# Performance work log

Measured on AMD Instinct MI355X. Metric: run time of the kernel, lower is better.

## Reference

```python
import jax, jax.numpy as jnp
import numpy as np

B, L, D = 32768, 256, 16  # batch, chain length, bond dim; physical dim d=2


def setup_inputs() -> dict:
    key = jax.random.key(0)
    k_phi, k_first, k_mid, k_last = jax.random.split(key, 4)
    scale = 1.0 / np.sqrt(2.0 * D)  # variance-preserving chain
    phi_batch = jax.random.normal(k_phi, (B, L, 2), dtype=jnp.float32)
    core_first = jax.random.normal(k_first, (2, D), dtype=jnp.float32) * scale
    cores_mid = jax.random.normal(k_mid, (L - 2, D, 2, D), dtype=jnp.float32) * scale
    core_last = jax.random.normal(k_last, (D, 2), dtype=jnp.float32) * scale
    out_bias = jnp.zeros((), dtype=jnp.float32)
    return {
        "phi_batch": phi_batch,
        "core_first": core_first,
        "cores_mid": cores_mid,
        "core_last": core_last,
        "out_bias": out_bias,
    }


def reference(phi_batch, core_first, cores_mid, core_last, out_bias):
    # MPS / tensor-train contraction, batched over samples.
    # Each sample contracts feature vectors phi[i] (len-2) into the physical
    # index of core i, then chains the resulting D x D matrices via a
    # left-to-right bond-space matvec (what cotengra would find per-sample).
    # v0: [B, D] = phi[:,0] contracted with first core [2, D]
    v0 = jnp.einsum("bp,pd->bd", phi_batch[:, 0], core_first)

    # middle features, scan-major layout: [L-2, B, 2]
    phis_mid = jnp.swapaxes(phi_batch[:, 1:-1], 0, 1)

    def step(v, xs):
        phi_t, core = xs  # phi_t: [B, 2], core: [D, 2, D]
        # contract bond then physical index; never materialize [B, D, D]
        u = jnp.einsum("bq,qpr->bpr", v, core)   # [B, 2, D]
        v_new = jnp.einsum("bp,bpr->br", phi_t, u)  # [B, D]
        return v_new, None

    v, _ = jax.lax.scan(step, v0, (phis_mid, cores_mid))

    # close the chain with last core [D, 2] and last feature [B, 2]
    out = jnp.einsum("bq,qp,bp->b", v, core_last, phi_batch[:, -1])
    return out + out_bias
```

## Files before the change

### kernel.cpp

```cpp
#include <hip/hip_runtime.h>
#include <stdint.h>


typedef short  bf16x8 __attribute__((ext_vector_type(8)));
typedef float  f32x4  __attribute__((ext_vector_type(4)));
typedef int    i32x4  __attribute__((ext_vector_type(4)));
typedef unsigned int u32;

#define NPF 64
#define NPB 63
#define BWD_OFF (NPF*4*64)
#define NCHUNK 32

#define PACK_HI(hi, lo) ((int)__builtin_amdgcn_perm((u32)(hi), (u32)(lo), 0x07060302u))

__device__ __forceinline__ u32 rne_bump(u32 u){ return u + 0x7FFFu + ((u >> 16) & 1u); }

__device__ __forceinline__ void async16(const void* g, void* l){
  __builtin_amdgcn_global_load_lds(
    (const __attribute__((address_space(1))) u32*)(uintptr_t)g,
    (__attribute__((address_space(3))) u32*)(uintptr_t)l, 16, 0, 0);
}

__global__ void build_pair_frags(const float* __restrict__ cm, i32x4* __restrict__ ws)
{
  __shared__ float Ca[512], Cb[512];
  const int bid = blockIdx.x;
  const bool fwd = bid < NPF;
  const int j  = fwd ? bid : bid - NPF;
  const int ta = fwd ? 2*j     : 252 - 2*j;
  const int tb = fwd ? 2*j + 1 : 253 - 2*j;
  {
    const float* A = cm + ta*512;
    const float* B = cm + tb*512;
    for (int i = threadIdx.x; i < 512; i += 256){ Ca[i] = A[i]; Cb[i] = B[i]; }
  }
  __syncthreads();
  const int f    = threadIdx.x >> 6;
  const int lane = threadIdx.x & 63;
  const int m    = lane & 15;
  const int g    = lane >> 4;
  const int p    = f >> 1, q = f & 1;
  u32 hi[4], lo[4];
  #pragma unroll
  for (int x = 0; x < 4; ++x){
    const int cq = 4*g + x;
    float acc = 0.f;
    #pragma unroll
    for (int r = 0; r < 16; ++r){
      const float a = fwd ? Ca[cq*32 + p*16 + r] : Ca[m*32 + p*16 + r];
      const float b = fwd ? Cb[r*32 + q*16 + m]  : Cb[r*32 + q*16 + cq];
      acc = fmaf(a, b, acc);
    }
    const u32 u  = __float_as_uint(acc);
    const u32 aa = rne_bump(u);
    const float hf = __uint_as_float(aa & 0xFFFF0000u);
    const u32 bb = rne_bump(__float_as_uint(acc - hf));
    hi[x] = aa >> 16; lo[x] = bb >> 16;
  }
  i32x4 w;
  w[0] = (int)(hi[0] | (hi[1] << 16));
  w[1] = (int)(hi[2] | (hi[3] << 16));
  w[2] = (int)(lo[0] | (lo[1] << 16));
  w[3] = (int)(lo[2] | (lo[3] << 16));
  ws[(fwd ? 0 : BWD_OFF) + (j*4 + f)*64 + lane] = w;
}

__global__ __launch_bounds__(256, 4) void mps_chain(
  const float* __restrict__ phi,
  const float* __restrict__ core_first,
  const float* __restrict__ core_last,
  const float* __restrict__ bias,
  const i32x4* __restrict__ ws,
  float* __restrict__ out)
{
  const int lane = threadIdx.x & 63;
  const int wv   = threadIdx.x >> 6;
  const int b0   = blockIdx.x * 32;
  const int n    = lane & 15;
  const int g    = lane >> 4;
  const int half = wv & 1;
  const int s_in = half*16 + n;
  const bool isFwd = (wv < 2);
  const int dirIdx = isFwd ? 0 : 1;

  __shared__ i32x4 frag[2][2][2][4][64];
  __shared__ float phL[2][2][2][4][16][4];

  const float* phiRow = phi + (size_t)(b0 + s_in) * 512;

  const float* phiDma = phi + (size_t)(b0 + 16*half + (lane & 15)) * 512
                            + (lane >> 4) * 4;
  const i32x4* wsD = isFwd ? ws : (ws + BWD_OFF);

  auto issue_dma = [&](int cn, int buf){
    int pr = 2*cn + half;
    if (!isFwd && pr > NPB-1) pr = NPB-1;
    const i32x4* base = wsD + pr*4*64 + lane;
    #pragma unroll
    for (int f = 0; f < 4; ++f)
      async16(base + f*64, &frag[dirIdx][buf][half][f][0]);
    const int W = isFwd ? 4*cn : (248 - 4*cn);
    async16(phiDma + 2*W, &phL[dirIdx][buf][half][0][0][0]);
  };

  float v[4];
  i32x4 bfr;

  auto make_bfrag = [&](){
    const u32 u0 = __float_as_uint(v[0]), u1 = __float_as_uint(v[1]);
    const u32 u2 = __float_as_uint(v[2]), u3 = __float_as_uint(v[3]);
    const float l0 = v[0] - __uint_as_float(u0 & 0xFFFF0000u);
    const float l1 = v[1] - __uint_as_float(u1 & 0xFFFF0000u);
    const float l2 = v[2] - __uint_as_float(u2 & 0xFFFF0000u);
    const float l3 = v[3] - __uint_as_float(u3 & 0xFFFF0000u);
    bfr[0] = PACK_HI(u1, u0);
    bfr[1] = PACK_HI(u3, u2);
    bfr[2] = PACK_HI(__float_as_uint(l1), __float_as_uint(l0));
    bfr[3] = PACK_HI(__float_as_uint(l3), __float_as_uint(l2));
  };

  auto pair_step = [&](const i32x4& G0, const i32x4& G1, const i32x4& G2,
                       const i32x4& G3, float2 cA, float2 cB){
    const float c00 = cA.x*cB.x, c01 = cA.x*cB.y;
    const float c10 = cA.y*cB.x, c11 = cA.y*cB.y;
    i32x4 sw; sw[0]=bfr[2]; sw[1]=bfr[3]; sw[2]=bfr[0]; sw[3]=bfr[1];
    const bf16x8 bh = __builtin_bit_cast(bf16x8, bfr);
    const bf16x8 bs = __builtin_bit_cast(bf16x8, sw);
    const f32x4 z = {0.f,0.f,0.f,0.f};
    f32x4 a00 = __builtin_amdgcn_mfma_f32_16x16x32_bf16(__builtin_bit_cast(bf16x8,G0), bh, z, 0,0,0);
    a00 = __builtin_amdgcn_mfma_f32_16x16x32_bf16(__builtin_bit_cast(bf16x8,G0), bs, a00, 0,0,0);
    f32x4 a01 = __builtin_amdgcn_mfma_f32_16x16x32_bf16(__builtin_bit_cast(bf16x8,G1), bh, z, 0,0,0);
    a01 = __builtin_amdgcn_mfma_f32_16x16x32_bf16(__builtin_bit_cast(bf16x8,G1), bs, a01, 0,0,0);
    f32x4 a10 = __builtin_amdgcn_mfma_f32_16x16x32_bf16(__builtin_bit_cast(bf16x8,G2), bh, z, 0,0,0);
    a10 = __builtin_amdgcn_mfma_f32_16x16x32_bf16(__builtin_bit_cast(bf16x8,G2), bs, a10, 0,0,0);
    f32x4 a11 = __builtin_amdgcn_mfma_f32_16x16x32_bf16(__builtin_bit_cast(bf16x8,G3), bh, z, 0,0,0);
    a11 = __builtin_amdgcn_mfma_f32_16x16x32_bf16(__builtin_bit_cast(bf16x8,G3), bs, a11, 0,0,0);
    #pragma unroll
    for (int i2 = 0; i2 < 4; ++i2)
      v[i2] = c00*a00[i2] + c01*a01[i2] + c10*a10[i2] + c11*a11[i2];
    make_bfrag();
  };

  if (isFwd){
    const float2 ph0 = *(const float2*)phiRow;
    #pragma unroll
    for (int reg = 0; reg < 4; ++reg){
      const int r = g*4 + reg;
      v[reg] = ph0.x * core_first[r] + ph0.y * core_first[16 + r];
    }
  } else {
    const float2 phL2 = *(const float2*)(phiRow + 510);
    #pragma unroll
    for (int reg = 0; reg < 4; ++reg){
      const int r = g*4 + reg;
      v[reg] = phL2.x * core_last[2*r] + phL2.y * core_last[2*r + 1];
    }
  }
  make_bfrag();

  issue_dma(0, 0);
  __syncthreads();

  #pragma unroll 1
  for (int c = 0; c < NCHUNK; ++c){
    const int buf = c & 1;
    if (c + 1 < NCHUNK) issue_dma(c + 1, buf ^ 1);

    const float* pb = &phL[dirIdx][buf][half][0][n][0];
    const float2 xA0 = *(const float2*)(pb + (isFwd ?   2 : 130));
    const float2 xB0 = *(const float2*)(pb + (isFwd ?  64 : 192));
    const float2 xA1 = *(const float2*)(pb + 66);
    const float2 xB1 = *(const float2*)(pb + 128);

    {
      const i32x4 G0 = frag[dirIdx][buf][0][0][lane];
      const i32x4 G1 = frag[dirIdx][buf][0][1][lane];
      const i32x4 G2 = frag[dirIdx][buf][0][2][lane];
      const i32x4 G3 = frag[dirIdx][buf][0][3][lane];
      pair_step(G0, G1, G2, G3, xA0, xB0);
    }
    if (isFwd || (2*c + 1) < NPB){
      const i32x4 G0 = frag[dirIdx][buf][1][0][lane];
      const i32x4 G1 = frag[dirIdx][buf][1][1][lane];
      const i32x4 G2 = frag[dirIdx][buf][1][2][lane];
      const i32x4 G3 = frag[dirIdx][buf][1][3][lane];
      pair_step(G0, G1, G2, G3, xA1, xB1);
    }
    __syncthreads();
  }

  float* red = (float*)&frag[0][0][0][0][0];
  *(float4*)&red[(dirIdx*32 + s_in)*20 + 4*g] =
      make_float4(v[0], v[1], v[2], v[3]);
  __syncthreads();
  if (threadIdx.x < 32){
    const int s = threadIdx.x;
    float acc = bias[0];
    #pragma unroll
    for (int qq = 0; qq < 16; ++qq)
      acc += red[s*20 + qq] * red[(32 + s)*20 + qq];
    out[b0 + s] = acc;
  }
}

extern "C" void kernel_launch(void* const* d_in, const int* in_sizes, int n_in,
                              void* d_out, int out_size, void* d_ws, size_t ws_size,
                              hipStream_t stream)
{
  const float* phi  = (const float*)d_in[0];
  const float* cf   = (const float*)d_in[1];
  const float* cm   = (const float*)d_in[2];
  const float* cl   = (const float*)d_in[3];
  const float* bias = (const float*)d_in[4];
  i32x4* ws = (i32x4*)d_ws;

  build_pair_frags<<<NPF + NPB, 256, 0, stream>>>(cm, ws);
  mps_chain<<<1024, 256, 0, stream>>>(phi, cf, cl, bias, ws, (float*)d_out);
}
```

Before: 138.0 us.

## Load phi features directly to registers with two-stage prefetch and manual waitcnt

Removes the LDS staging buffer for phi features. Each lane now reads float4 phi values straight from global memory into registers, prefetched two chunks ahead, with a carry register handling the odd/even feature alignment. The pair-fragment DMA becomes a simple pointer walk, and the workspace is padded with extra pairs so that overrun reads stay in bounds. The full __syncthreads is replaced by an explicit vmcnt waitcnt plus s_barrier so the register prefetches can remain in flight across iterations. The trade-offs are fragile hand-written waitcnt encodings, extra build blocks that read cores outside their valid range, and more register pressure.

New measurement: 143.1 us. 1.04x slower.

```diff
diff --git a/kernel.cpp b/kernel.cpp
--- a/kernel.cpp
+++ b/kernel.cpp
@@ -9,7 +9,8 @@
 
 #define NPF 64
 #define NPB 63
-#define BWD_OFF (NPF*4*64)
+#define NP_ALLOC 66
+#define BWD_OFF (NP_ALLOC*4*64)
 #define NCHUNK 32
 
 #define PACK_HI(hi, lo) ((int)__builtin_amdgcn_perm((u32)(hi), (u32)(lo), 0x07060302u))
@@ -26,8 +27,8 @@
 {
   __shared__ float Ca[512], Cb[512];
   const int bid = blockIdx.x;
-  const bool fwd = bid < NPF;
-  const int j  = fwd ? bid : bid - NPF;
+  const bool fwd = bid < NP_ALLOC;
+  const int j  = fwd ? bid : bid - NP_ALLOC;
   const int ta = fwd ? 2*j     : 252 - 2*j;
   const int tb = fwd ? 2*j + 1 : 253 - 2*j;
   {
@@ -85,27 +86,17 @@
   const int dirIdx = isFwd ? 0 : 1;
 
   __shared__ i32x4 frag[2][2][2][4][64];
-  __shared__ float phL[2][2][2][4][16][4];
 
   const float* phiRow = phi + (size_t)(b0 + s_in) * 512;
-
-  const float* phiDma = phi + (size_t)(b0 + 16*half + (lane & 15)) * 512
-                            + (lane >> 4) * 4;
   const i32x4* wsD = isFwd ? ws : (ws + BWD_OFF);
 
-  auto issue_dma = [&](int cn, int buf){
-    int pr = 2*cn + half;
-    if (!isFwd && pr > NPB-1) pr = NPB-1;
-    const i32x4* base = wsD + pr*4*64 + lane;
-    #pragma unroll
-    for (int f = 0; f < 4; ++f)
-      async16(base + f*64, &frag[dirIdx][buf][half][f][0]);
-    const int W = isFwd ? 4*cn : (248 - 4*cn);
-    async16(phiDma + 2*W, &phL[dirIdx][buf][half][0][0][0]);
-  };
+  const i32x4* dmaSrc = wsD + half*256 + lane;
+  i32x4* const dst0 = &frag[dirIdx][0][half][0][0];
+  i32x4* const dst1 = &frag[dirIdx][1][half][0][0];
 
   float v[4];
   i32x4 bfr;
+  const f32x4 z = {0.f,0.f,0.f,0.f};
 
   auto make_bfrag = [&](){
     const u32 u0 = __float_as_uint(v[0]), u1 = __float_as_uint(v[1]);
@@ -120,14 +111,13 @@
     bfr[3] = PACK_HI(__float_as_uint(l3), __float_as_uint(l2));
   };
 
-  auto pair_step = [&](const i32x4& G0, const i32x4& G1, const i32x4& G2,
-                       const i32x4& G3, float2 cA, float2 cB){
+  auto pair_step = [&](const i32x4* fr, float2 cA, float2 cB){
+    const i32x4 G0 = fr[0], G1 = fr[64], G2 = fr[128], G3 = fr[192];
     const float c00 = cA.x*cB.x, c01 = cA.x*cB.y;
     const float c10 = cA.y*cB.x, c11 = cA.y*cB.y;
     i32x4 sw; sw[0]=bfr[2]; sw[1]=bfr[3]; sw[2]=bfr[0]; sw[3]=bfr[1];
     const bf16x8 bh = __builtin_bit_cast(bf16x8, bfr);
     const bf16x8 bs = __builtin_bit_cast(bf16x8, sw);
-    const f32x4 z = {0.f,0.f,0.f,0.f};
     f32x4 a00 = __builtin_amdgcn_mfma_f32_16x16x32_bf16(__builtin_bit_cast(bf16x8,G0), bh, z, 0,0,0);
     a00 = __builtin_amdgcn_mfma_f32_16x16x32_bf16(__builtin_bit_cast(bf16x8,G0), bs, a00, 0,0,0);
     f32x4 a01 = __builtin_amdgcn_mfma_f32_16x16x32_bf16(__builtin_bit_cast(bf16x8,G1), bh, z, 0,0,0);
@@ -137,59 +127,83 @@
     f32x4 a11 = __builtin_amdgcn_mfma_f32_16x16x32_bf16(__builtin_bit_cast(bf16x8,G3), bh, z, 0,0,0);
     a11 = __builtin_amdgcn_mfma_f32_16x16x32_bf16(__builtin_bit_cast(bf16x8,G3), bs, a11, 0,0,0);
     #pragma unroll
-    for (int i2 = 0; i2 < 4; ++i2)
-      v[i2] = c00*a00[i2] + c01*a01[i2] + c10*a10[i2] + c11*a11[i2];
+    for (int i2 = 0; i2 < 4; ++i2){
+      float t = c00*a00[i2];
+      t = fmaf(c01, a01[i2], t);
+      t = fmaf(c10, a10[i2], t);
+      t = fmaf(c11, a11[i2], t);
+      v[i2] = t;
+    }
     make_bfrag();
   };
 
+  const int initOff = isFwd ? 0 : 508;
+  const float4 L0 = *(const float4*)(phiRow + initOff);
   if (isFwd){
-    const float2 ph0 = *(const float2*)phiRow;
     #pragma unroll
     for (int reg = 0; reg < 4; ++reg){
       const int r = g*4 + reg;
-      v[reg] = ph0.x * core_first[r] + ph0.y * core_first[16 + r];
+      v[reg] = L0.x * core_first[r] + L0.y * core_first[16 + r];
     }
   } else {
-    const float2 phL2 = *(const float2*)(phiRow + 510);
     #pragma unroll
     for (int reg = 0; reg < 4; ++reg){
       const int r = g*4 + reg;
-      v[reg] = phL2.x * core_last[2*r] + phL2.y * core_last[2*r + 1];
+      v[reg] = L0.z * core_last[2*r] + L0.w * core_last[2*r + 1];
     }
   }
   make_bfrag();
-
-  issue_dma(0, 0);
-  __syncthreads();
+  float2 carry = isFwd ? make_float2(L0.z, L0.w) : make_float2(L0.x, L0.y);
+
+  const int offA = isFwd ? 4 : 504;
+  const int offB = isFwd ? 8 : 500;
+  const int dph  = isFwd ? 8 : -8;
+
+  {
+    #pragma unroll
+    for (int f = 0; f < 4; ++f) async16(dmaSrc + f*64, dst0 + f*64);
+  }
+  float4 A_cur = *(const float4*)(phiRow + offA);
+  float4 B_cur = *(const float4*)(phiRow + offB);
+  float4 A_nxt = *(const float4*)(phiRow + offA + dph);
+  float4 B_nxt = *(const float4*)(phiRow + offB + dph);
+  __builtin_amdgcn_s_waitcnt(0x3F74);
+  __builtin_amdgcn_s_barrier();
+
+  const i32x4* dmaS = dmaSrc + 512;
 
   #pragma unroll 1
   for (int c = 0; c < NCHUNK; ++c){
-    const int buf = c & 1;
-    if (c + 1 < NCHUNK) issue_dma(c + 1, buf ^ 1);
-
-    const float* pb = &phL[dirIdx][buf][half][0][n][0];
-    const float2 xA0 = *(const float2*)(pb + (isFwd ?   2 : 130));
-    const float2 xB0 = *(const float2*)(pb + (isFwd ?  64 : 192));
-    const float2 xA1 = *(const float2*)(pb + 66);
-    const float2 xB1 = *(const float2*)(pb + 128);
-
-    {
-      const i32x4 G0 = frag[dirIdx][buf][0][0][lane];
-      const i32x4 G1 = frag[dirIdx][buf][0][1][lane];
-      const i32x4 G2 = frag[dirIdx][buf][0][2][lane];
-      const i32x4 G3 = frag[dirIdx][buf][0][3][lane];
-      pair_step(G0, G1, G2, G3, xA0, xB0);
-    }
-    if (isFwd || (2*c + 1) < NPB){
-      const i32x4 G0 = frag[dirIdx][buf][1][0][lane];
-      const i32x4 G1 = frag[dirIdx][buf][1][1][lane];
-      const i32x4 G2 = frag[dirIdx][buf][1][2][lane];
-      const i32x4 G3 = frag[dirIdx][buf][1][3][lane];
-      pair_step(G0, G1, G2, G3, xA1, xB1);
-    }
-    __syncthreads();
-  }
-
+    i32x4* dst = (c & 1) ? dst0 : dst1;
+    #pragma unroll
+    for (int f = 0; f < 4; ++f) async16(dmaS + f*64, dst + f*64);
+    dmaS += 512;
+
+    const float4 A_in = *(const float4*)(phiRow + offA + (c+2)*dph);
+    const float4 B_in = *(const float4*)(phiRow + offB + (c+2)*dph);
+
+    float2 cA0, cB0, cA1, cB1;
+    if (isFwd){
+      cA0 = carry;                        cB0 = make_float2(A_cur.x, A_cur.y);
+      cA1 = make_float2(A_cur.z, A_cur.w); cB1 = make_float2(B_cur.x, B_cur.y);
+      carry = make_float2(B_cur.z, B_cur.w);
+    } else {
+      cA0 = make_float2(A_cur.z, A_cur.w); cB0 = carry;
+      cA1 = make_float2(B_cur.z, B_cur.w); cB1 = make_float2(A_cur.x, A_cur.y);
+      carry = make_float2(B_cur.x, B_cur.y);
+    }
+    const i32x4* rd = &frag[dirIdx][c & 1][0][0][lane];
+    pair_step(rd, cA0, cB0);
+    if (isFwd || (2*c + 1) < NPB)
+      pair_step(rd + 256, cA1, cB1);
+
+    A_cur = A_nxt; B_cur = B_nxt; A_nxt = A_in; B_nxt = B_in;
+
+    __builtin_amdgcn_s_waitcnt(0x3F72);
+    __builtin_amdgcn_s_barrier();
+  }
+
+  __syncthreads();
   float* red = (float*)&frag[0][0][0][0][0];
   *(float4*)&red[(dirIdx*32 + s_in)*20 + 4*g] =
       make_float4(v[0], v[1], v[2], v[3]);
@@ -215,6 +229,6 @@
   const float* bias = (const float*)d_in[4];
   i32x4* ws = (i32x4*)d_ws;
 
-  build_pair_frags<<<NPF + NPB, 256, 0, stream>>>(cm, ws);
+  build_pair_frags<<<2*NP_ALLOC, 256, 0, stream>>>(cm, ws);
   mps_chain<<<1024, 256, 0, stream>>>(phi, cf, cl, bias, ws, (float*)d_out);
 }
```
